# Performance work log

Measured on AMD Instinct MI355X. Metric: run time of the kernel, lower is better.

The kernel has to match this reference:

```python
import jax, jax.numpy as jnp
import numpy as np

BATCH = 8192
N_FEATURES = 512
DEPTH = 10
N_LEAVES = 2 ** DEPTH
ATOMS = N_FEATURES + 1  # include_one=True
TAU = 1.0


def eml(a, b):
    # Assumed definition of the custom binary eml op: smooth-max / log-sum-exp.
    # eml(a, b) = log(exp(a) + exp(b)), computed stably.
    return jnp.logaddexp(a, b)


def setup_inputs() -> dict:
    key = jax.random.key(0)
    k1, k2 = jax.random.split(key)
    X = jax.random.normal(k1, (BATCH, N_FEATURES), dtype=jnp.float32)
    leaf_logits = jax.random.normal(k2, (N_LEAVES, ATOMS), dtype=jnp.float32) * 0.1
    return {"X": X, "leaf_logits": leaf_logits}


def reference(X, leaf_logits):
    batch = X.shape[0]
    # atom values: prepend constant 1 (include_one=True) -> (batch, atoms)
    atom_values = jnp.concatenate([jnp.ones((batch, 1), dtype=X.dtype), X], axis=1)
    # softmax over atoms per leaf, then mix: (batch, n_leaves)
    weights = jax.nn.softmax(leaf_logits / TAU, axis=-1)
    current = jnp.einsum('ba,la->bl', atom_values, weights)
    # binary tree reduction: log2(n_leaves) steps over strided slices
    while current.shape[-1] > 1:
        current = eml(current[..., 0::2], current[..., 1::2])
    return current.squeeze(-1)  # (batch,)
```

## Files before the change

### kernel.cpp

```cpp
#include <hip/hip_runtime.h>
#include <hip/hip_bf16.h>

#define BATCH 8192
#define NF 512
#define NL 1024
#define ATOMS 513

typedef float float4v __attribute__((ext_vector_type(4)));
typedef int int4v __attribute__((ext_vector_type(4)));
typedef long long2v __attribute__((ext_vector_type(2)));

__device__ __forceinline__ unsigned char f2fp8(float x) {
    return (unsigned char)(__builtin_amdgcn_cvt_pk_fp8_f32(x, x, 0, false) & 0xff);
}

__device__ __forceinline__ void load_lds16(const void* g, void* ldsbase) {
    __builtin_amdgcn_global_load_lds(
        (const __attribute__((address_space(1))) unsigned int*)g,
        (__attribute__((address_space(3))) unsigned int*)ldsbase,
        16, 0, 0);
}


#define N_CONVERT_BLOCKS 512
#define N_SOFTMAX_BLOCKS 1024

__global__ void prep_kernel(const float* __restrict__ X,
                            const float* __restrict__ logits,
                            unsigned char* __restrict__ Xp,
                            unsigned char* __restrict__ Wp,
                            float* __restrict__ bias) {
    int bi = blockIdx.x;
    int t  = threadIdx.x;

    if (bi < N_CONVERT_BLOCKS) {
        __shared__ unsigned char tile[16 * 512];
        int rt = bi;
        const float* base = X + (size_t)rt * 16 * 512;
#pragma unroll
        for (int i = 0; i < 8; ++i) {
            float4v v = *reinterpret_cast<const float4v*>(base + (size_t)i * 1024 + t * 4);
            int w = __builtin_amdgcn_cvt_pk_fp8_f32(v[0], v[1], 0, false);
            w = __builtin_amdgcn_cvt_pk_fp8_f32(v[2], v[3], w, true);
            reinterpret_cast<int*>(tile)[i * 256 + t] = w;
        }
        __syncthreads();
        int kp = t >> 5, j = t & 31;
#pragma unroll
        for (int e = 0; e < 2; ++e) {
            int ln = 2 * j + e;
            int l16 = ln & 15, quad = ln >> 4;
            const int* s0 = reinterpret_cast<const int*>(tile + l16 * 512 + (2 * kp) * 32 + quad * 8);
            const int* s1 = reinterpret_cast<const int*>(tile + l16 * 512 + (2 * kp + 1) * 32 + quad * 8);
            int4v o = (int4v){s0[0], s0[1], s1[0], s1[1]};
            *reinterpret_cast<int4v*>(Xp + (((size_t)rt * 8 + kp) * 64 + ln) * 16) = o;
        }
        return;
    }

    int l = bi - N_CONVERT_BLOCKS;
    int wave = t >> 6, lane = t & 63;
    const float* row = logits + (size_t)l * ATOMS;
    float v0 = row[t];
    float v1 = row[t + 256];
    float v2 = (t == 0) ? row[512] : -1e30f;

    __shared__ float red[8];
    float m = fmaxf(fmaxf(v0, v1), v2);
#pragma unroll
    for (int o = 32; o > 0; o >>= 1) m = fmaxf(m, __shfl_xor(m, o, 64));
    if (lane == 0) red[wave] = m;
    __syncthreads();
    float mx = fmaxf(fmaxf(red[0], red[1]), fmaxf(red[2], red[3]));

    float e0 = __expf(v0 - mx);
    float e1 = __expf(v1 - mx);
    float e2 = (t == 0) ? __expf(v2 - mx) : 0.f;
    float s = e0 + e1 + e2;
#pragma unroll
    for (int o = 32; o > 0; o >>= 1) s += __shfl_xor(s, o, 64);
    if (lane == 0) red[4 + wave] = s;
    __syncthreads();
    float inv = 1.f / (red[4] + red[5] + red[6] + red[7]);
    float inv512 = inv * 512.f;

    auto wp_off = [](int l_, int k_) -> size_t {
        int lt = l_ >> 4, l16_ = l_ & 15;
        int ks = k_ >> 5, kp_ = ks >> 1, half = ks & 1;
        int quad_ = (k_ >> 3) & 3, byt = k_ & 7;
        return ((size_t)((lt * 8 + kp_) * 64) + quad_ * 16 + l16_) * 16 + half * 8 + byt;
    };

    if (t == 0) {
        bias[l] = e0 * inv;
        Wp[wp_off(l, 511)] = f2fp8(e2 * inv512);
    } else {
        Wp[wp_off(l, t - 1)] = f2fp8(e0 * inv512);
    }
    Wp[wp_off(l, t + 255)] = f2fp8(e1 * inv512);
}

__global__ __launch_bounds__(256, 2)
void gemm_lse_kernel(const unsigned char* __restrict__ Xp,
                     const unsigned char* __restrict__ Wp,
                     const float* __restrict__ bias,
                     float* __restrict__ partial) {
    __shared__ unsigned char Bl[64 * 1024];
    __shared__ float sums[128];

    int tid  = threadIdx.x;
    int wave = tid >> 6;
    int lane = tid & 63;
    int quad = lane >> 4;
    int l16  = lane & 15;

    int lg  = blockIdx.x & 7;
    int rsb = blockIdx.x >> 3;

    {
        const unsigned char* gb = Wp + (size_t)lg * 65536 + wave * 16384 + lane * 16;
        unsigned char* lb = Bl + wave * 16384;
#pragma unroll
        for (int j = 0; j < 16; ++j)
            load_lds16(gb + j * 1024, lb + j * 1024);
    }

    const unsigned char* pa = Xp + ((size_t)(rsb * 8 + wave * 2) * 8) * 1024 + lane * 16;

    float4v acc[2][8];
#pragma unroll
    for (int mt = 0; mt < 2; ++mt)
#pragma unroll
        for (int nt = 0; nt < 8; ++nt)
            acc[mt][nt] = (float4v){0.f, 0.f, 0.f, 0.f};

    __syncthreads();

#pragma unroll
    for (int kp = 0; kp < 8; ++kp) {
        long2v af[2], bf[8];
#pragma unroll
        for (int mt = 0; mt < 2; ++mt)
            af[mt] = *reinterpret_cast<const long2v*>(pa + (size_t)mt * 8192 + kp * 1024);
#pragma unroll
        for (int nt = 0; nt < 8; ++nt)
            bf[nt] = *reinterpret_cast<const long2v*>(Bl + (nt * 8 + kp) * 1024 + lane * 16);

#pragma unroll
        for (int mt = 0; mt < 2; ++mt)
#pragma unroll
            for (int nt = 0; nt < 8; ++nt) {
                acc[mt][nt] = __builtin_amdgcn_mfma_f32_16x16x32_fp8_fp8(
                    af[mt][0], bf[nt][0], acc[mt][nt], 0, 0, 0);
                acc[mt][nt] = __builtin_amdgcn_mfma_f32_16x16x32_fp8_fp8(
                    af[mt][1], bf[nt][1], acc[mt][nt], 0, 0, 0);
            }
    }

    float bl[8];
#pragma unroll
    for (int nt = 0; nt < 8; ++nt)
        bl[nt] = bias[lg * 128 + nt * 16 + l16];

    const float INV512 = 0.001953125f;
    float ps[2][4];
#pragma unroll
    for (int mt = 0; mt < 2; ++mt)
#pragma unroll
        for (int r = 0; r < 4; ++r) ps[mt][r] = 0.f;

#pragma unroll
    for (int nt = 0; nt < 8; ++nt)
#pragma unroll
        for (int mt = 0; mt < 2; ++mt)
#pragma unroll
            for (int r = 0; r < 4; ++r)
                ps[mt][r] += __expf(fmaf(acc[mt][nt][r], INV512, bl[nt]));

#pragma unroll
    for (int m = 1; m < 16; m <<= 1)
#pragma unroll
        for (int mt = 0; mt < 2; ++mt)
#pragma unroll
            for (int r = 0; r < 4; ++r)
                ps[mt][r] += __shfl_xor(ps[mt][r], m, 64);

    if (l16 == 0) {
#pragma unroll
        for (int mt = 0; mt < 2; ++mt)
#pragma unroll
            for (int r = 0; r < 4; ++r)
                sums[wave * 32 + mt * 16 + quad * 4 + r] = ps[mt][r];
    }
    __syncthreads();
    if (tid < 128)
        partial[(size_t)lg * BATCH + rsb * 128 + tid] = sums[tid];
}

__global__ void combine_kernel(const float* __restrict__ partial,
                               float* __restrict__ out) {
    int i = blockIdx.x * 256 + threadIdx.x;
    float s = 0.f;
#pragma unroll
    for (int c = 0; c < 8; ++c) s += partial[(size_t)c * BATCH + i];
    out[i] = logf(s);
}

extern "C" void kernel_launch(void* const* d_in, const int* in_sizes, int n_in,
                              void* d_out, int out_size, void* d_ws, size_t ws_size,
                              hipStream_t stream) {
    const float* X      = (const float*)d_in[0];
    const float* logits = (const float*)d_in[1];
    float* out = (float*)d_out;

    char* ws = (char*)d_ws;
    unsigned char* Xp = (unsigned char*)ws;
    unsigned char* Wp = (unsigned char*)(ws + (size_t)BATCH * NF);
    float* bias = (float*)(ws + (size_t)BATCH * NF + (size_t)NL * NF);
    float* part = (float*)((char*)bias + NL * sizeof(float));

    prep_kernel<<<N_CONVERT_BLOCKS + N_SOFTMAX_BLOCKS, 256, 0, stream>>>(X, logits, Xp, Wp, bias);
    gemm_lse_kernel<<<(BATCH / 128) * (NL / 128), 256, 0, stream>>>(Xp, Wp, bias, part);
    combine_kernel<<<BATCH / 256, 256, 0, stream>>>(part, out);
}
```

Baseline: 78.62 us.

## Fuse combine kernel into GEMM via atomic accumulation and last-block finalize

Removes the separate combine kernel: each GEMM block atomically adds its partial sum-exp into a per-row buffer, and the last of the 8 column-group blocks for a row tile (found with an atomic counter) takes the log and writes the output. The prep kernel gains extra blocks that zero the accumulators and counters. The bias load is also hoisted ahead of the MFMA loop. This saves one kernel launch and the partial buffer round trip, but adds atomic traffic and relies on relaxed atomics for ordering between blocks, and floating-point summation order is no longer deterministic.

Result: no change. 78.49 us (-0.2%).

```diff
diff --git a/kernel.cpp b/kernel.cpp
--- a/kernel.cpp
+++ b/kernel.cpp
@@ -24,12 +24,15 @@
 
 #define N_CONVERT_BLOCKS 512
 #define N_SOFTMAX_BLOCKS 1024
+#define N_ZERO_BLOCKS    33
 
 __global__ void prep_kernel(const float* __restrict__ X,
                             const float* __restrict__ logits,
                             unsigned char* __restrict__ Xp,
                             unsigned char* __restrict__ Wp,
-                            float* __restrict__ bias) {
+                            float* __restrict__ bias,
+                            float* __restrict__ sumexp,
+                            int* __restrict__ cnt) {
     int bi = blockIdx.x;
     int t  = threadIdx.x;
 
@@ -58,55 +61,65 @@
         return;
     }
 
-    int l = bi - N_CONVERT_BLOCKS;
-    int wave = t >> 6, lane = t & 63;
-    const float* row = logits + (size_t)l * ATOMS;
-    float v0 = row[t];
-    float v1 = row[t + 256];
-    float v2 = (t == 0) ? row[512] : -1e30f;
-
-    __shared__ float red[8];
-    float m = fmaxf(fmaxf(v0, v1), v2);
-#pragma unroll
-    for (int o = 32; o > 0; o >>= 1) m = fmaxf(m, __shfl_xor(m, o, 64));
-    if (lane == 0) red[wave] = m;
-    __syncthreads();
-    float mx = fmaxf(fmaxf(red[0], red[1]), fmaxf(red[2], red[3]));
-
-    float e0 = __expf(v0 - mx);
-    float e1 = __expf(v1 - mx);
-    float e2 = (t == 0) ? __expf(v2 - mx) : 0.f;
-    float s = e0 + e1 + e2;
-#pragma unroll
-    for (int o = 32; o > 0; o >>= 1) s += __shfl_xor(s, o, 64);
-    if (lane == 0) red[4 + wave] = s;
-    __syncthreads();
-    float inv = 1.f / (red[4] + red[5] + red[6] + red[7]);
-    float inv512 = inv * 512.f;
-
-    auto wp_off = [](int l_, int k_) -> size_t {
-        int lt = l_ >> 4, l16_ = l_ & 15;
-        int ks = k_ >> 5, kp_ = ks >> 1, half = ks & 1;
-        int quad_ = (k_ >> 3) & 3, byt = k_ & 7;
-        return ((size_t)((lt * 8 + kp_) * 64) + quad_ * 16 + l16_) * 16 + half * 8 + byt;
-    };
-
-    if (t == 0) {
-        bias[l] = e0 * inv;
-        Wp[wp_off(l, 511)] = f2fp8(e2 * inv512);
-    } else {
-        Wp[wp_off(l, t - 1)] = f2fp8(e0 * inv512);
-    }
-    Wp[wp_off(l, t + 255)] = f2fp8(e1 * inv512);
+    if (bi < N_CONVERT_BLOCKS + N_SOFTMAX_BLOCKS) {
+        int l = bi - N_CONVERT_BLOCKS;
+        int wave = t >> 6, lane = t & 63;
+        const float* row = logits + (size_t)l * ATOMS;
+        float v0 = row[t];
+        float v1 = row[t + 256];
+        float v2 = (t == 0) ? row[512] : -1e30f;
+
+        __shared__ float red[8];
+        float m = fmaxf(fmaxf(v0, v1), v2);
+#pragma unroll
+        for (int o = 32; o > 0; o >>= 1) m = fmaxf(m, __shfl_xor(m, o, 64));
+        if (lane == 0) red[wave] = m;
+        __syncthreads();
+        float mx = fmaxf(fmaxf(red[0], red[1]), fmaxf(red[2], red[3]));
+
+        float e0 = __expf(v0 - mx);
+        float e1 = __expf(v1 - mx);
+        float e2 = (t == 0) ? __expf(v2 - mx) : 0.f;
+        float s = e0 + e1 + e2;
+#pragma unroll
+        for (int o = 32; o > 0; o >>= 1) s += __shfl_xor(s, o, 64);
+        if (lane == 0) red[4 + wave] = s;
+        __syncthreads();
+        float inv = 1.f / (red[4] + red[5] + red[6] + red[7]);
+        float inv512 = inv * 512.f;
+
+        auto wp_off = [](int l_, int k_) -> size_t {
+            int lt = l_ >> 4, l16_ = l_ & 15;
+            int ks = k_ >> 5, kp_ = ks >> 1, half = ks & 1;
+            int quad_ = (k_ >> 3) & 3, byt = k_ & 7;
+            return ((size_t)((lt * 8 + kp_) * 64) + quad_ * 16 + l16_) * 16 + half * 8 + byt;
+        };
+
+        if (t == 0) {
+            bias[l] = e0 * inv;
+            Wp[wp_off(l, 511)] = f2fp8(e2 * inv512);
+        } else {
+            Wp[wp_off(l, t - 1)] = f2fp8(e0 * inv512);
+        }
+        Wp[wp_off(l, t + 255)] = f2fp8(e1 * inv512);
+        return;
+    }
+
+    int i = (bi - N_CONVERT_BLOCKS - N_SOFTMAX_BLOCKS) * 256 + t;
+    if (i < BATCH) sumexp[i] = 0.f;
+    else { int j = i - BATCH; if (j < 64) cnt[j] = 0; }
 }
 
 __global__ __launch_bounds__(256, 2)
 void gemm_lse_kernel(const unsigned char* __restrict__ Xp,
                      const unsigned char* __restrict__ Wp,
                      const float* __restrict__ bias,
-                     float* __restrict__ partial) {
+                     float* __restrict__ sumexp,
+                     int* __restrict__ cnt,
+                     float* __restrict__ out) {
     __shared__ unsigned char Bl[64 * 1024];
     __shared__ float sums[128];
+    __shared__ int lastFlag;
 
     int tid  = threadIdx.x;
     int wave = tid >> 6;
@@ -126,6 +139,11 @@
     }
 
     const unsigned char* pa = Xp + ((size_t)(rsb * 8 + wave * 2) * 8) * 1024 + lane * 16;
+
+    float bl[8];
+#pragma unroll
+    for (int nt = 0; nt < 8; ++nt)
+        bl[nt] = bias[lg * 128 + nt * 16 + l16];
 
     float4v acc[2][8];
 #pragma unroll
@@ -157,11 +175,6 @@
             }
     }
 
-    float bl[8];
-#pragma unroll
-    for (int nt = 0; nt < 8; ++nt)
-        bl[nt] = bias[lg * 128 + nt * 16 + l16];
-
     const float INV512 = 0.001953125f;
     float ps[2][4];
 #pragma unroll
@@ -193,17 +206,24 @@
                 sums[wave * 32 + mt * 16 + quad * 4 + r] = ps[mt][r];
     }
     __syncthreads();
+
     if (tid < 128)
-        partial[(size_t)lg * BATCH + rsb * 128 + tid] = sums[tid];
-}
-
-__global__ void combine_kernel(const float* __restrict__ partial,
-                               float* __restrict__ out) {
-    int i = blockIdx.x * 256 + threadIdx.x;
-    float s = 0.f;
-#pragma unroll
-    for (int c = 0; c < 8; ++c) s += partial[(size_t)c * BATCH + i];
-    out[i] = logf(s);
+        __hip_atomic_fetch_add(&sumexp[rsb * 128 + tid], sums[tid],
+                               __ATOMIC_RELAXED, __HIP_MEMORY_SCOPE_AGENT);
+    __syncthreads();
+
+    if (tid == 0) {
+        int old = __hip_atomic_fetch_add(&cnt[rsb], 1,
+                                         __ATOMIC_RELAXED, __HIP_MEMORY_SCOPE_AGENT);
+        lastFlag = (old == 7);
+    }
+    __syncthreads();
+
+    if (lastFlag && tid < 128) {
+        float s = __hip_atomic_fetch_add(&sumexp[rsb * 128 + tid], 0.0f,
+                                         __ATOMIC_RELAXED, __HIP_MEMORY_SCOPE_AGENT);
+        out[rsb * 128 + tid] = logf(s);
+    }
 }
 
 extern "C" void kernel_launch(void* const* d_in, const int* in_sizes, int n_in,
@@ -216,10 +236,12 @@
     char* ws = (char*)d_ws;
     unsigned char* Xp = (unsigned char*)ws;
     unsigned char* Wp = (unsigned char*)(ws + (size_t)BATCH * NF);
-    float* bias = (float*)(ws + (size_t)BATCH * NF + (size_t)NL * NF);
-    float* part = (float*)((char*)bias + NL * sizeof(float));
-
-    prep_kernel<<<N_CONVERT_BLOCKS + N_SOFTMAX_BLOCKS, 256, 0, stream>>>(X, logits, Xp, Wp, bias);
-    gemm_lse_kernel<<<(BATCH / 128) * (NL / 128), 256, 0, stream>>>(Xp, Wp, bias, part);
-    combine_kernel<<<BATCH / 256, 256, 0, stream>>>(part, out);
-}
+    float* bias   = (float*)(ws + (size_t)BATCH * NF + (size_t)NL * NF);
+    float* sumexp = (float*)((char*)bias + NL * sizeof(float));
+    int*   cnt    = (int*)((char*)sumexp + BATCH * sizeof(float));
+
+    prep_kernel<<<N_CONVERT_BLOCKS + N_SOFTMAX_BLOCKS + N_ZERO_BLOCKS, 256, 0, stream>>>(
+        X, logits, Xp, Wp, bias, sumexp, cnt);
+    gemm_lse_kernel<<<(BATCH / 128) * (NL / 128), 256, 0, stream>>>(
+        Xp, Wp, bias, sumexp, cnt, out);
+}
```
